# Performance work log

Measured on AMD Instinct MI355X. Metric: run time of the kernel, lower is better.

Reference implementation:

```python
import jax, jax.numpy as jnp
import numpy as np

N, C, H, W = 16, 128, 128, 128


def setup_inputs() -> dict:
    key = jax.random.key(0)
    ks = jax.random.split(key, 7)
    s = 0.02
    return {
        "x": jax.random.normal(ks[0], (N, C, H, W), dtype=jnp.float32),
        "w_key": jax.random.normal(ks[1], (C, C), dtype=jnp.float32) * s,
        "b_key": jax.random.normal(ks[2], (C,), dtype=jnp.float32) * s,
        "w_query": jax.random.normal(ks[3], (C, C), dtype=jnp.float32) * s,
        "b_query": jax.random.normal(ks[4], (C,), dtype=jnp.float32) * s,
        "w_value": jax.random.normal(ks[5], (C, C), dtype=jnp.float32) * s,
        "b_value": jax.random.normal(ks[6], (C,), dtype=jnp.float32) * s,
        "gamma": jnp.zeros((1,), dtype=jnp.float32),
    }


def _conv1x1(x, w, b):
    # 1x1 conv: (N,C,H,W) x (O,C) -> (N,O,H,W)
    return jnp.einsum('nchw,oc->nohw', x, w) + b[None, :, None, None]


def reference(x, w_key, b_key, w_query, b_query, w_value, b_value, gamma):
    k = _conv1x1(x, w_key, b_key)
    q = _conv1x1(x, w_query, b_query)
    v = _conv1x1(x, w_value, b_value)
    k_size = x.shape[1]  # output_channel
    scale = jnp.asarray(k_size, x.dtype) ** 0.5
    # similarity[n,o,w,v] = sum_h k[n,o,h,w] * q[n,o,h,v]  (k^T over H @ q)
    sim = jnp.einsum('nohw,nohv->nowv', k, q) / scale
    # softmax over dim=2 (the first W axis)
    attn = jax.nn.softmax(sim, axis=2)
    # out[n,o,h,v] = sum_w v[n,o,h,w] * attn[n,o,w,v]
    out = jnp.einsum('nohw,nowv->nohv', v, attn)
    return gamma[0] * out + x
```

## Files before the change

kernel.cpp:

```cpp
#include <hip/hip_runtime.h>
#include <hip/hip_bf16.h>
#include <math.h>

#define CN      128
#define HWN     16384
#define NBATCH  16
#define PLANE   (CN * HWN)
#define TSTRIDE ((size_t)NBATCH * PLANE)

typedef __attribute__((ext_vector_type(8))) short  short8;
typedef __attribute__((ext_vector_type(4))) float  float4v;

__device__ __forceinline__ unsigned short f2b(float f) {
    __hip_bfloat16 h = __float2bfloat16(f);
    return *reinterpret_cast<unsigned short*>(&h);
}
__device__ __forceinline__ unsigned packbf(float lo, float hi) {
    return (unsigned)f2b(lo) | ((unsigned)f2b(hi) << 16);
}
__device__ __forceinline__ float bf2f(unsigned short u) {
    union { unsigned i; float f; } x; x.i = ((unsigned)u) << 16; return x.f;
}

__global__ void prep_kernel(const float* __restrict__ wk, const float* __restrict__ bk,
                            const float* __restrict__ wq, const float* __restrict__ bq,
                            const float* __restrict__ wv, const float* __restrict__ bv,
                            unsigned short* __restrict__ wbf, float* __restrict__ bias)
{
    int i = blockIdx.x * 256 + threadIdx.x;
    int tensor = i >> 14, oc = i & 16383;
    const float* w = tensor == 0 ? wk : (tensor == 1 ? wq : wv);
    wbf[i] = f2b(w[oc]);
    if (i < 384) {
        const float* b = i < 128 ? bk : (i < 256 ? bq : bv);
        bias[i] = b[i & 127];
    }
}

__global__ __launch_bounds__(256) void kqv_kernel(
    const float* __restrict__ x, const unsigned short* __restrict__ wbf,
    const float* __restrict__ bias, unsigned short* __restrict__ kqv)
{
    __shared__ unsigned Xl[64 * 68];

    const int n   = blockIdx.y;
    const int hw0 = blockIdx.x * 64;
    const int t    = threadIdx.x;
    const int lane = t & 63, wv = t >> 6;
    const int l15  = lane & 15, quad = lane >> 4;

    const float* xp = x + (size_t)n * PLANE + hw0 + lane;
    #pragma unroll
    for (int it = 0; it < 4; ++it) {
        const int c0 = (wv * 4 + it) * 8;
        float v[8];
        #pragma unroll
        for (int j = 0; j < 8; ++j) v[j] = xp[(size_t)(c0 + j) * HWN];
        uint4 u;
        u.x = packbf(v[0], v[1]); u.y = packbf(v[2], v[3]);
        u.z = packbf(v[4], v[5]); u.w = packbf(v[6], v[7]);
        *(uint4*)&Xl[lane * 68 + c0 / 2] = u;
    }
    __syncthreads();

    short8 bfr[4][4];
    #pragma unroll
    for (int nt = 0; nt < 4; ++nt)
        #pragma unroll
        for (int k = 0; k < 4; ++k)
            bfr[nt][k] = *(const short8*)&Xl[(nt * 16 + l15) * 68 + quad * 4 + k * 16];

    for (int mt = 0; mt < 6; ++mt) {
        const int o0 = wv * 96 + mt * 16;
        short8 afr[4];
        #pragma unroll
        for (int k = 0; k < 4; ++k)
            afr[k] = *(const short8*)&wbf[(o0 + l15) * CN + quad * 8 + k * 32];
        float b0 = bias[o0 + quad * 4 + 0], b1 = bias[o0 + quad * 4 + 1];
        float b2 = bias[o0 + quad * 4 + 2], b3 = bias[o0 + quad * 4 + 3];

        #pragma unroll
        for (int nt = 0; nt < 4; ++nt) {
            float4v acc = {b0, b1, b2, b3};
            #pragma unroll
            for (int k = 0; k < 4; ++k)
                acc = __builtin_amdgcn_mfma_f32_16x16x32_bf16(afr[k], bfr[nt][k], acc, 0, 0, 0);
            #pragma unroll
            for (int r = 0; r < 4; ++r) {
                const int oo = o0 + quad * 4 + r;
                const size_t idx = (size_t)(oo >> 7) * TSTRIDE
                                 + ((size_t)n * CN + (oo & 127)) * HWN
                                 + hw0 + nt * 16 + l15;
                kqv[idx] = f2b(acc[r]);
            }
        }
    }
}

__global__ __launch_bounds__(256) void attn_kernel(
    const unsigned short* __restrict__ kqv, const float* __restrict__ x,
    const float* __restrict__ gamma, float* __restrict__ out)
{
    __shared__ unsigned lds[17408];
    unsigned* Kt = lds;
    unsigned* Qt = lds + 8704;
    unsigned short* At = (unsigned short*)lds;

    const int no = blockIdx.x;
    const unsigned short* Kg = kqv + (size_t)no * HWN;
    const unsigned short* Qg = Kg + TSTRIDE;
    const unsigned short* Vg = Kg + 2 * TSTRIDE;

    const int t = threadIdx.x, lane = t & 63, wv = t >> 6;
    const int l15 = lane & 15, quad = lane >> 4;

    #pragma unroll
    for (int p = 0; p < 8; ++p) {
        const int w  = (p & 1) * 64 + lane;
        const int h0 = ((p >> 1) * 4 + wv) * 8;
        unsigned short kv[8], qv[8];
        #pragma unroll
        for (int j = 0; j < 8; ++j) {
            kv[j] = Kg[(h0 + j) * 128 + w];
            qv[j] = Qg[(h0 + j) * 128 + w];
        }
        uint4 a, b;
        a.x = (unsigned)kv[0] | ((unsigned)kv[1] << 16); a.y = (unsigned)kv[2] | ((unsigned)kv[3] << 16);
        a.z = (unsigned)kv[4] | ((unsigned)kv[5] << 16); a.w = (unsigned)kv[6] | ((unsigned)kv[7] << 16);
        b.x = (unsigned)qv[0] | ((unsigned)qv[1] << 16); b.y = (unsigned)qv[2] | ((unsigned)qv[3] << 16);
        b.z = (unsigned)qv[4] | ((unsigned)qv[5] << 16); b.w = (unsigned)qv[6] | ((unsigned)qv[7] << 16);
        *(uint4*)&Kt[w * 68 + h0 / 2] = a;
        *(uint4*)&Qt[w * 68 + h0 / 2] = b;
    }
    __syncthreads();

    const int v0 = wv * 32;
    float4v acc1[2][8];
    #pragma unroll
    for (int mt = 0; mt < 2; ++mt)
        #pragma unroll
        for (int nt = 0; nt < 8; ++nt) acc1[mt][nt] = (float4v){0.f, 0.f, 0.f, 0.f};

    {
        short8 afr[2][4];
        #pragma unroll
        for (int mt = 0; mt < 2; ++mt)
            #pragma unroll
            for (int k = 0; k < 4; ++k)
                afr[mt][k] = *(const short8*)&Qt[(v0 + mt * 16 + l15) * 68 + quad * 4 + k * 16];
        #pragma unroll
        for (int nt = 0; nt < 8; ++nt) {
            short8 bfr[4];
            #pragma unroll
            for (int k = 0; k < 4; ++k)
                bfr[k] = *(const short8*)&Kt[(nt * 16 + l15) * 68 + quad * 4 + k * 16];
            #pragma unroll
            for (int mt = 0; mt < 2; ++mt)
                #pragma unroll
                for (int k = 0; k < 4; ++k)
                    acc1[mt][nt] = __builtin_amdgcn_mfma_f32_16x16x32_bf16(afr[mt][k], bfr[k], acc1[mt][nt], 0, 0, 0);
        }
    }
    __syncthreads();

    const float sc = 0.08838834764831845f;
    #pragma unroll
    for (int mt = 0; mt < 2; ++mt)
        #pragma unroll
        for (int r = 0; r < 4; ++r) {
            float m = -INFINITY;
            #pragma unroll
            for (int nt = 0; nt < 8; ++nt) {
                acc1[mt][nt][r] *= sc;
                m = fmaxf(m, acc1[mt][nt][r]);
            }
            #pragma unroll
            for (int d = 1; d < 16; d <<= 1) m = fmaxf(m, __shfl_xor(m, d, 64));
            float s = 0.f;
            #pragma unroll
            for (int nt = 0; nt < 8; ++nt) {
                const float e = __expf(acc1[mt][nt][r] - m);
                acc1[mt][nt][r] = e;
                s += e;
            }
            #pragma unroll
            for (int d = 1; d < 16; d <<= 1) s += __shfl_xor(s, d, 64);
            const float inv = 1.0f / s;
            const int v = v0 + mt * 16 + quad * 4 + r;
            #pragma unroll
            for (int nt = 0; nt < 8; ++nt)
                At[v * 136 + nt * 16 + l15] = f2b(acc1[mt][nt][r] * inv);
        }
    __syncthreads();

    const int h0 = wv * 32;
    float4v acc2[2][8];
    #pragma unroll
    for (int mt = 0; mt < 2; ++mt)
        #pragma unroll
        for (int nt = 0; nt < 8; ++nt) acc2[mt][nt] = (float4v){0.f, 0.f, 0.f, 0.f};

    {
        short8 vfr[2][4];
        #pragma unroll
        for (int mt = 0; mt < 2; ++mt)
            #pragma unroll
            for (int k = 0; k < 4; ++k)
                vfr[mt][k] = *(const short8*)&Vg[(h0 + mt * 16 + l15) * 128 + quad * 8 + k * 32];
        #pragma unroll
        for (int nt = 0; nt < 8; ++nt) {
            short8 bfr[4];
            #pragma unroll
            for (int k = 0; k < 4; ++k)
                bfr[k] = *(const short8*)&At[(nt * 16 + l15) * 136 + quad * 8 + k * 32];
            #pragma unroll
            for (int mt = 0; mt < 2; ++mt)
                #pragma unroll
                for (int k = 0; k < 4; ++k)
                    acc2[mt][nt] = __builtin_amdgcn_mfma_f32_16x16x32_bf16(vfr[mt][k], bfr[k], acc2[mt][nt], 0, 0, 0);
        }
    }

    const float g = gamma[0];
    const float* xp = x + (size_t)no * HWN;
    float*       op = out + (size_t)no * HWN;
    #pragma unroll
    for (int mt = 0; mt < 2; ++mt)
        #pragma unroll
        for (int nt = 0; nt < 8; ++nt)
            #pragma unroll
            for (int r = 0; r < 4; ++r) {
                const int h = h0 + mt * 16 + quad * 4 + r;
                const int v = nt * 16 + l15;
                const int idx = h * 128 + v;
                op[idx] = fmaf(g, acc2[mt][nt][r], xp[idx]);
            }
}

extern "C" void kernel_launch(void* const* d_in, const int* in_sizes, int n_in,
                              void* d_out, int out_size, void* d_ws, size_t ws_size,
                              hipStream_t stream) {
    const float* x     = (const float*)d_in[0];
    const float* wk    = (const float*)d_in[1];
    const float* bk    = (const float*)d_in[2];
    const float* wq    = (const float*)d_in[3];
    const float* bq    = (const float*)d_in[4];
    const float* wv    = (const float*)d_in[5];
    const float* bv    = (const float*)d_in[6];
    const float* gamma = (const float*)d_in[7];
    float* out = (float*)d_out;

    unsigned short* wbf  = (unsigned short*)d_ws;
    float*          bias = (float*)((char*)d_ws + (192 << 10));
    unsigned short* kqv  = (unsigned short*)((char*)d_ws + (256 << 10));

    prep_kernel<<<192, 256, 0, stream>>>(wk, bk, wq, bq, wv, bv, wbf, bias);
    dim3 gA(HWN / 64, NBATCH);
    kqv_kernel<<<gA, 256, 0, stream>>>(x, wbf, bias, kqv);
    attn_kernel<<<NBATCH * CN, 256, 0, stream>>>(kqv, x, gamma, out);
}
```

Measured before the change: 428.8 us.

## Vectorize global loads/stores by swapping MFMA operand roles in both kernels

In the projection kernel, x is read with float4 loads. The MFMA A/B operands are swapped so each lane's four accumulator values are contiguous along hw, which allows packed 8-byte bf16 stores to kqv. In the attention kernel, each wave now computes output rows matching its own softmax rows (v0), so the barrier between softmax and the PV matmul is removed. Output and residual accesses become float4. The aim is fewer, wider memory transactions and one less block-wide sync, at the cost of more complex fragment indexing.

```diff
diff --git a/kernel.cpp b/kernel.cpp
--- a/kernel.cpp
+++ b/kernel.cpp
@@ -17,9 +17,6 @@
 }
 __device__ __forceinline__ unsigned packbf(float lo, float hi) {
     return (unsigned)f2b(lo) | ((unsigned)f2b(hi) << 16);
-}
-__device__ __forceinline__ float bf2f(unsigned short u) {
-    union { unsigned i; float f; } x; x.i = ((unsigned)u) << 16; return x.f;
 }
 
 __global__ void prep_kernel(const float* __restrict__ wk, const float* __restrict__ bk,
@@ -49,50 +46,55 @@
     const int lane = t & 63, wv = t >> 6;
     const int l15  = lane & 15, quad = lane >> 4;
 
-    const float* xp = x + (size_t)n * PLANE + hw0 + lane;
-    #pragma unroll
-    for (int it = 0; it < 4; ++it) {
-        const int c0 = (wv * 4 + it) * 8;
-        float v[8];
-        #pragma unroll
-        for (int j = 0; j < 8; ++j) v[j] = xp[(size_t)(c0 + j) * HWN];
-        uint4 u;
-        u.x = packbf(v[0], v[1]); u.y = packbf(v[2], v[3]);
-        u.z = packbf(v[4], v[5]); u.w = packbf(v[6], v[7]);
-        *(uint4*)&Xl[lane * 68 + c0 / 2] = u;
+    {
+        const int hwg = (t & 15) * 4;
+        const int c0  = (t >> 4) * 8;
+        const float* xp = x + (size_t)n * PLANE + (size_t)c0 * HWN + hw0 + hwg;
+        float v[8][4];
+        #pragma unroll
+        for (int j = 0; j < 8; ++j)
+            *(float4*)v[j] = *(const float4*)(xp + (size_t)j * HWN);
+        #pragma unroll
+        for (int jj = 0; jj < 4; ++jj) {
+            uint4 u;
+            u.x = packbf(v[0][jj], v[1][jj]);
+            u.y = packbf(v[2][jj], v[3][jj]);
+            u.z = packbf(v[4][jj], v[5][jj]);
+            u.w = packbf(v[6][jj], v[7][jj]);
+            *(uint4*)&Xl[(hwg + jj) * 68 + c0 / 2] = u;
+        }
     }
     __syncthreads();
 
-    short8 bfr[4][4];
-    #pragma unroll
-    for (int nt = 0; nt < 4; ++nt)
+    short8 afr[4][4];
+    #pragma unroll
+    for (int mt = 0; mt < 4; ++mt)
         #pragma unroll
         for (int k = 0; k < 4; ++k)
-            bfr[nt][k] = *(const short8*)&Xl[(nt * 16 + l15) * 68 + quad * 4 + k * 16];
-
-    for (int mt = 0; mt < 6; ++mt) {
-        const int o0 = wv * 96 + mt * 16;
-        short8 afr[4];
+            afr[mt][k] = *(const short8*)&Xl[(mt * 16 + l15) * 68 + quad * 4 + k * 16];
+
+    #pragma unroll
+    for (int nt = 0; nt < 6; ++nt) {
+        const int ob = wv * 96 + nt * 16;
+        const int tensor = ob >> 7;
+        const int oc = (ob & 127) + l15;
+        short8 wfr[4];
         #pragma unroll
         for (int k = 0; k < 4; ++k)
-            afr[k] = *(const short8*)&wbf[(o0 + l15) * CN + quad * 8 + k * 32];
-        float b0 = bias[o0 + quad * 4 + 0], b1 = bias[o0 + quad * 4 + 1];
-        float b2 = bias[o0 + quad * 4 + 2], b3 = bias[o0 + quad * 4 + 3];
-
-        #pragma unroll
-        for (int nt = 0; nt < 4; ++nt) {
-            float4v acc = {b0, b1, b2, b3};
-            #pragma unroll
-            for (int k = 0; k < 4; ++k)
-                acc = __builtin_amdgcn_mfma_f32_16x16x32_bf16(afr[k], bfr[nt][k], acc, 0, 0, 0);
-            #pragma unroll
-            for (int r = 0; r < 4; ++r) {
-                const int oo = o0 + quad * 4 + r;
-                const size_t idx = (size_t)(oo >> 7) * TSTRIDE
-                                 + ((size_t)n * CN + (oo & 127)) * HWN
-                                 + hw0 + nt * 16 + l15;
-                kqv[idx] = f2b(acc[r]);
-            }
+            wfr[k] = *(const short8*)&wbf[(ob + l15) * CN + quad * 8 + k * 32];
+        const float b = bias[ob + l15];
+        unsigned short* dst = kqv + (size_t)tensor * TSTRIDE
+                            + ((size_t)n * CN + oc) * HWN + hw0 + quad * 4;
+        #pragma unroll
+        for (int mt = 0; mt < 4; ++mt) {
+            float4v acc = {b, b, b, b};
+            #pragma unroll
+            for (int k = 0; k < 4; ++k)
+                acc = __builtin_amdgcn_mfma_f32_16x16x32_bf16(afr[mt][k], wfr[k], acc, 0, 0, 0);
+            uint2 u;
+            u.x = packbf(acc[0], acc[1]);
+            u.y = packbf(acc[2], acc[3]);
+            *(uint2*)(dst + mt * 16) = u;
         }
     }
 }
@@ -191,9 +193,7 @@
             for (int nt = 0; nt < 8; ++nt)
                 At[v * 136 + nt * 16 + l15] = f2b(acc1[mt][nt][r] * inv);
         }
-    __syncthreads();
-
-    const int h0 = wv * 32;
+
     float4v acc2[2][8];
     #pragma unroll
     for (int mt = 0; mt < 2; ++mt)
@@ -201,23 +201,23 @@
         for (int nt = 0; nt < 8; ++nt) acc2[mt][nt] = (float4v){0.f, 0.f, 0.f, 0.f};
 
     {
-        short8 vfr[2][4];
+        short8 pfr[2][4];
         #pragma unroll
         for (int mt = 0; mt < 2; ++mt)
             #pragma unroll
             for (int k = 0; k < 4; ++k)
-                vfr[mt][k] = *(const short8*)&Vg[(h0 + mt * 16 + l15) * 128 + quad * 8 + k * 32];
+                pfr[mt][k] = *(const short8*)&At[(v0 + mt * 16 + l15) * 136 + quad * 8 + k * 32];
         #pragma unroll
         for (int nt = 0; nt < 8; ++nt) {
-            short8 bfr[4];
-            #pragma unroll
-            for (int k = 0; k < 4; ++k)
-                bfr[k] = *(const short8*)&At[(nt * 16 + l15) * 136 + quad * 8 + k * 32];
+            short8 vfr[4];
+            #pragma unroll
+            for (int k = 0; k < 4; ++k)
+                vfr[k] = *(const short8*)&Vg[(nt * 16 + l15) * 128 + quad * 8 + k * 32];
             #pragma unroll
             for (int mt = 0; mt < 2; ++mt)
                 #pragma unroll
                 for (int k = 0; k < 4; ++k)
-                    acc2[mt][nt] = __builtin_amdgcn_mfma_f32_16x16x32_bf16(vfr[mt][k], bfr[k], acc2[mt][nt], 0, 0, 0);
+                    acc2[mt][nt] = __builtin_amdgcn_mfma_f32_16x16x32_bf16(pfr[mt][k], vfr[k], acc2[mt][nt], 0, 0, 0);
         }
     }
 
@@ -227,14 +227,18 @@
     #pragma unroll
     for (int mt = 0; mt < 2; ++mt)
         #pragma unroll
-        for (int nt = 0; nt < 8; ++nt)
-            #pragma unroll
-            for (int r = 0; r < 4; ++r) {
-                const int h = h0 + mt * 16 + quad * 4 + r;
-                const int v = nt * 16 + l15;
-                const int idx = h * 128 + v;
-                op[idx] = fmaf(g, acc2[mt][nt][r], xp[idx]);
-            }
+        for (int nt = 0; nt < 8; ++nt) {
+            const int h    = nt * 16 + l15;
+            const int vcol = v0 + mt * 16 + quad * 4;
+            const int idx  = h * 128 + vcol;
+            float4 xv = *(const float4*)(xp + idx);
+            float4 ov;
+            ov.x = fmaf(g, acc2[mt][nt][0], xv.x);
+            ov.y = fmaf(g, acc2[mt][nt][1], xv.y);
+            ov.z = fmaf(g, acc2[mt][nt][2], xv.z);
+            ov.w = fmaf(g, acc2[mt][nt][3], xv.w);
+            *(float4*)(op + idx) = ov;
+        }
 }
 
 extern "C" void kernel_launch(void* const* d_in, const int* in_sizes, int n_in,
```

Measured after the change: 443.5 us. 1.03x slower.
